# Kernel tuning notes

Hardware: AMD Instinct MI355X
Metric: run time of the kernel (lower is better)

Reference implementation:

```python
import jax, jax.numpy as jnp
import numpy as np
from jax import lax

K = 40
EPS = 1e-5
SLOPE = 0.2


def knn_idx(x, k):
    # x: (B, C, N); returns (B, N, k) indices of k nearest (L2), self included
    xx = jnp.sum(x * x, axis=1)                      # (B, N)
    inner = jnp.einsum('bcn,bcm->bnm', x, x)         # (B, N, N)
    dist = xx[:, :, None] - 2.0 * inner + xx[:, None, :]
    _, idx = lax.top_k(-dist, k)
    return idx


def get_graph_feature(x, k):
    # x: (B, C, N) -> (B, 2C, N, k)
    idx = knn_idx(x, k)
    xt = jnp.transpose(x, (0, 2, 1))                 # (B, N, C)
    feat = jax.vmap(lambda t, i: t[i])(xt, idx)      # (B, N, k, C)
    center = xt[:, :, None, :]                       # (B, N, 1, C)
    e = jnp.concatenate([feat - center, jnp.broadcast_to(center, feat.shape)], axis=-1)
    return jnp.transpose(e, (0, 3, 1, 2))            # (B, 2C, N, k)


def edge_block(x, W, gamma, beta, k):
    # EdgeConv: graph feature -> 1x1 conv -> BN(train-mode) -> LeakyReLU -> max over k
    e = get_graph_feature(x, k)                      # (B, 2C, N, k)
    y = jnp.einsum('oc,bcnk->bonk', W, e)            # (B, 32, N, k)
    m = jnp.mean(y, axis=(0, 2, 3), keepdims=True)
    v = jnp.mean((y - m) ** 2, axis=(0, 2, 3), keepdims=True)
    y = (y - m) / jnp.sqrt(v + EPS)
    y = y * gamma[None, :, None, None] + beta[None, :, None, None]
    y = jnp.where(y >= 0, y, SLOPE * y)
    return jnp.max(y, axis=-1)                       # (B, 32, N)


def setup_inputs() -> dict:
    key = jax.random.key(0)
    ks = jax.random.split(key, 16)
    B, C, N = 8, 9, 2048
    d = {
        'x': jax.random.normal(ks[0], (B, C, N), jnp.float32),
        'W1': jax.random.normal(ks[1], (32, 18), jnp.float32) * 0.1,
        'W2': jax.random.normal(ks[2], (32, 64), jnp.float32) * 0.1,
        'W3': jax.random.normal(ks[3], (32, 64), jnp.float32) * 0.1,
        'W4': jax.random.normal(ks[4], (32, 64), jnp.float32) * 0.1,
        'W5': jax.random.normal(ks[5], (128, 128), jnp.float32) * 0.1,
    }
    for i in range(4):
        d[f'g{i+1}'] = jnp.ones((32,), jnp.float32)
        d[f'b{i+1}'] = jnp.zeros((32,), jnp.float32)
    return d


def reference(x, W1, W2, W3, W4, W5, g1, g2, g3, g4, b1, b2, b3, b4):
    x1 = edge_block(x, W1, g1, b1, K)
    x2 = edge_block(x1, W2, g2, b2, K) + x1
    x3 = edge_block(x2, W3, g3, b3, K) + x2
    x4 = edge_block(x3, W4, g4, b4, K) + x3
    cat = jnp.concatenate([x1, x2, x3, x4], axis=1)  # (B, 128, N)
    return jnp.einsum('oc,bcn->bon', W5, cat)        # (B, 128, N)
```

## Files before the change

### kernel.cpp

```cpp
#include <hip/hip_runtime.h>
#include <stdint.h>

#define NP 2048
#define KNN 40
#define CAP 128

__device__ __forceinline__ unsigned fOrd(float f) {
    unsigned u = __float_as_uint(f);
    return u ^ ((unsigned)((int)u >> 31) | 0x80000000u);
}
__device__ __forceinline__ unsigned long long dOrd(double d) {
    unsigned long long u = (unsigned long long)__double_as_longlong(d);
    return u ^ (((unsigned long long)((long long)u >> 63)) | 0x8000000000000000ull);
}

template<int C, int CP, int CPX>
__global__ void prep_kernel(const float* __restrict__ X, long bstride,
                            const float* __restrict__ W,
                            float* __restrict__ p, float* __restrict__ r,
                            float* __restrict__ xx, float* __restrict__ XT) {
    __shared__ float wdT[C][32];
    __shared__ float wrT[C][32];
    int tid = threadIdx.x;
    for (int i = tid; i < 32 * C; i += 256) {
        int o = i / C, c = i - o * C;
        float wd = W[o * 2 * C + c];
        float wc = W[o * 2 * C + C + c];
        wdT[c][o] = wd;
        wrT[c][o] = wc - wd;
    }
    __syncthreads();
    int lane = tid & 63;
    int o = lane & 31;
    int h = lane >> 5;
    int wv = tid >> 6;
    int flat = blockIdx.x * 8 + wv * 2 + h;
    int b = flat >> 11, n = flat & 2047;
    const float* Xb = X + (long)b * bstride + n;
    float pacc = 0.f, racc = 0.f, xxa = 0.f, xto = 0.f;
    double xxd = 0.0;
#pragma unroll
    for (int c = 0; c < C; c++) {
        float xv = Xb[(long)c * NP];
        pacc = fmaf(wdT[c][o], xv, pacc);
        racc = fmaf(wrT[c][o], xv, racc);
        xxa += xv * xv;
        xxd += (double)xv * (double)xv;
        if (c == o) xto = xv;
    }
    long base = ((long)b * NP + n) * 32 + o;
    p[base] = pacc;
    r[base] = racc;
    long rowb = ((long)b * NP + n) * CPX;
    if (o < CP) XT[rowb + o] = (o < C) ? xto : 0.f;
    if (o == 0) {
        xx[b * NP + n] = xxa;
        *reinterpret_cast<double*>(&XT[rowb + CP]) = xxd;
    }
}

template<int C, int CP, int CPX>
__global__ __launch_bounds__(256, 2)
void knn_kernel(const float* __restrict__ X, long bstride,
                const float* __restrict__ p, const float* __restrict__ r,
                const float* __restrict__ xx, const float* __restrict__ XT,
                float* __restrict__ mmax, float* __restrict__ mmin,
                float* __restrict__ sums) {
    __shared__ __align__(16) float xt[2][C * 128];
    __shared__ __align__(16) float xxt[256];
    __shared__ __align__(8) float qld[4][CP][2];
    __shared__ int sel[8][KNN];
    __shared__ int cand[8][CAP];
    __shared__ float S1loc[32], S2loc[32];
    int tid = threadIdx.x;
    if (tid < 32) { S1loc[tid] = 0.f; S2loc[tid] = 0.f; }
    for (int i = tid; i < 8 * KNN; i += 256) ((int*)sel)[i] = 0;
    int lane = tid & 63;
    int wv = tid >> 6;
    int half = lane >> 5;
    int l32 = lane & 31;
    int b = blockIdx.x >> 8;
    int n0 = (blockIdx.x & 255) * 8;
    int nA = n0 + wv * 2, nB = nA + 1;
    int rowA = wv * 2, rowB = rowA + 1;
    const float* Xb = X + (long)b * bstride;
    const float* XTb = XT + (long)b * NP * CPX;
    long bNP = (long)b * NP;

    if (lane < CP) {
        qld[wv][lane][0] = XTb[(long)nA * CPX + lane];
        qld[wv][lane][1] = XTb[(long)nB * CPX + lane];
    }
    float xxnA = xx[bNP + nA];
    float xxnB = xx[bNP + nB];

    unsigned uA[16], uB[16];
    for (int t2 = 0; t2 < 8; t2++) {
        __syncthreads();
        for (int i = tid; i < C * 64; i += 256) {
            int c = i >> 6, g = i & 63;
            int tt = g >> 5, gg = g & 31;
            *(float4*)&xt[tt][c * 128 + gg * 4] =
                *(const float4*)&Xb[(long)c * NP + (t2 * 2 + tt) * 128 + gg * 4];
        }
        xxt[tid] = xx[bNP + t2 * 256 + tid];
        __syncthreads();
        const float* xth = xt[half];
        float4 ia = make_float4(0.f, 0.f, 0.f, 0.f);
        float4 ib = make_float4(0.f, 0.f, 0.f, 0.f);
#pragma unroll
        for (int c = 0; c < C; c++) {
            float2 q = *(const float2*)&qld[wv][c][0];
            float4 xv = *(const float4*)&xth[c * 128 + 4 * l32];
            ia.x = fmaf(q.x, xv.x, ia.x);
            ia.y = fmaf(q.x, xv.y, ia.y);
            ia.z = fmaf(q.x, xv.z, ia.z);
            ia.w = fmaf(q.x, xv.w, ia.w);
            ib.x = fmaf(q.y, xv.x, ib.x);
            ib.y = fmaf(q.y, xv.y, ib.y);
            ib.z = fmaf(q.y, xv.z, ib.z);
            ib.w = fmaf(q.y, xv.w, ib.w);
        }
        float4 xm = *(const float4*)&xxt[half * 128 + 4 * l32];
        unsigned a0 = fOrd((xxnA - 2.0f * ia.x) + xm.x) >> 16;
        unsigned a1 = fOrd((xxnA - 2.0f * ia.y) + xm.y) >> 16;
        unsigned a2 = fOrd((xxnA - 2.0f * ia.z) + xm.z) >> 16;
        unsigned a3 = fOrd((xxnA - 2.0f * ia.w) + xm.w) >> 16;
        unsigned b0 = fOrd((xxnB - 2.0f * ib.x) + xm.x) >> 16;
        unsigned b1 = fOrd((xxnB - 2.0f * ib.y) + xm.y) >> 16;
        unsigned b2_ = fOrd((xxnB - 2.0f * ib.z) + xm.z) >> 16;
        unsigned b3 = fOrd((xxnB - 2.0f * ib.w) + xm.w) >> 16;
        uA[2 * t2]     = (a1 << 16) | a0;
        uA[2 * t2 + 1] = (a3 << 16) | a2;
        uB[2 * t2]     = (b1 << 16) | b0;
        uB[2 * t2 + 1] = (b3 << 16) | b2_;
    }

    unsigned long long lmlt = (1ull << lane) - 1ull;

    double xxdA = *reinterpret_cast<const double*>(&XTb[(long)nA * CPX + CP]);
    double xxdB = *reinterpret_cast<const double*>(&XTb[(long)nB * CPX + CP]);

    unsigned vA = 0u, vB = 0u;
    for (int bit = 15; bit >= 0; bit--) {
        unsigned tA = vA | ((1u << bit) - 1u);
        unsigned tB = vB | ((1u << bit) - 1u);
        int cA = 0, cB = 0;
#pragma unroll
        for (int t = 0; t < 16; t++) {
            cA += __popcll(__ballot((uA[t] & 0xFFFFu) <= tA));
            cA += __popcll(__ballot((uA[t] >> 16) <= tA));
            cB += __popcll(__ballot((uB[t] & 0xFFFFu) <= tB));
            cB += __popcll(__ballot((uB[t] >> 16) <= tB));
        }
        if (cA < KNN) vA |= (1u << bit);
        if (cB < KNN) vB |= (1u << bit);
    }
    unsigned thrA = (vA > 0xFFFEu) ? 0xFFFFu : vA + 1u;
    unsigned thrB = (vB > 0xFFFEu) ? 0xFFFFu : vB + 1u;

    int baseA = 0, baseB = 0;
#pragma unroll
    for (int kk = 0; kk < 16; kk++) {
#pragma unroll
        for (int hh = 0; hh < 2; hh++) {
            unsigned kA = hh ? (uA[kk] >> 16) : (uA[kk] & 0xFFFFu);
            unsigned kB = hh ? (uB[kk] >> 16) : (uB[kk] & 0xFFFFu);
            int idx = (kk >> 1) * 256 + half * 128 + 4 * l32 + (kk & 1) * 2 + hh;
            bool pA = (kA <= thrA), pB = (kB <= thrB);
            unsigned long long mkA = __ballot(pA), mkB = __ballot(pB);
            if (pA) {
                int pos = baseA + __popcll(mkA & lmlt);
                if (pos < CAP) cand[rowA][pos] = idx;
            }
            if (pB) {
                int pos = baseB + __popcll(mkB & lmlt);
                if (pos < CAP) cand[rowB][pos] = idx;
            }
            baseA += __popcll(mkA);
            baseB += __popcll(mkB);
        }
    }
    int cntA = baseA < CAP ? baseA : CAP;
    int cntB = baseB < CAP ? baseB : CAP;

    unsigned long long keyA[CAP / 64], keyB[CAP / 64];
    int mixA[CAP / 64], mixB[CAP / 64];
#pragma unroll
    for (int s3 = 0; s3 < CAP / 64; s3++) {
        int slot = s3 * 64 + lane;
        keyA[s3] = ~0ull; mixA[s3] = 0;
        keyB[s3] = ~0ull; mixB[s3] = 0;
        if (slot < cntA) {
            int m = cand[rowA][slot] & (NP - 1);
            mixA[s3] = m;
            const float* xmp = XTb + (long)m * CPX;
            double inner = 0.0;
#pragma unroll
            for (int g = 0; g < CP / 4; g++) {
                float4 v = *(const float4*)&xmp[g * 4];
                inner += (double)qld[wv][g * 4 + 0][0] * (double)v.x;
                inner += (double)qld[wv][g * 4 + 1][0] * (double)v.y;
                inner += (double)qld[wv][g * 4 + 2][0] * (double)v.z;
                inner += (double)qld[wv][g * 4 + 3][0] * (double)v.w;
            }
            double xxm = *reinterpret_cast<const double*>(&xmp[CP]);
            double dd = (xxdA - 2.0 * inner) + xxm;
            keyA[s3] = dOrd(dd);
        }
        if (slot < cntB) {
            int m = cand[rowB][slot] & (NP - 1);
            mixB[s3] = m;
            const float* xmp = XTb + (long)m * CPX;
            double inner = 0.0;
#pragma unroll
            for (int g = 0; g < CP / 4; g++) {
                float4 v = *(const float4*)&xmp[g * 4];
                inner += (double)qld[wv][g * 4 + 0][1] * (double)v.x;
                inner += (double)qld[wv][g * 4 + 1][1] * (double)v.y;
                inner += (double)qld[wv][g * 4 + 2][1] * (double)v.z;
                inner += (double)qld[wv][g * 4 + 3][1] * (double)v.w;
            }
            double xxm = *reinterpret_cast<const double*>(&xmp[CP]);
            double dd = (xxdB - 2.0 * inner) + xxm;
            keyB[s3] = dOrd(dd);
        }
    }

    unsigned long long VA = 0ull, VB = 0ull;
    for (int bit = 62; bit >= 0; bit -= 2) {
        unsigned long long low = (1ull << bit) - 1ull;
        unsigned long long tA0 = VA | low;
        unsigned long long tA1 = VA | (1ull << bit) | low;
        unsigned long long tA2 = VA | (2ull << bit) | low;
        unsigned long long tB0 = VB | low;
        unsigned long long tB1 = VB | (1ull << bit) | low;
        unsigned long long tB2 = VB | (2ull << bit) | low;
        int cA0 = 0, cA1 = 0, cA2 = 0, cB0 = 0, cB1 = 0, cB2 = 0;
#pragma unroll
        for (int s3 = 0; s3 < CAP / 64; s3++) {
            cA0 += __popcll(__ballot(keyA[s3] <= tA0));
            cA1 += __popcll(__ballot(keyA[s3] <= tA1));
            cA2 += __popcll(__ballot(keyA[s3] <= tA2));
            cB0 += __popcll(__ballot(keyB[s3] <= tB0));
            cB1 += __popcll(__ballot(keyB[s3] <= tB1));
            cB2 += __popcll(__ballot(keyB[s3] <= tB2));
        }
        if (cA0 >= KNN) {  }
        else if (cA1 >= KNN) VA |= (1ull << bit);
        else if (cA2 >= KNN) VA |= (2ull << bit);
        else VA |= (3ull << bit);
        if (cB0 >= KNN) {  }
        else if (cB1 >= KNN) VB |= (1ull << bit);
        else if (cB2 >= KNN) VB |= (2ull << bit);
        else VB |= (3ull << bit);
    }

    int b2A = 0, b2B = 0;
#pragma unroll
    for (int s3 = 0; s3 < CAP / 64; s3++) {
        bool pA = (keyA[s3] < VA);
        bool pB = (keyB[s3] < VB);
        unsigned long long mkA = __ballot(pA), mkB = __ballot(pB);
        if (pA) {
            int pos = b2A + __popcll(mkA & lmlt);
            if (pos < KNN) sel[rowA][pos] = mixA[s3];
        }
        if (pB) {
            int pos = b2B + __popcll(mkB & lmlt);
            if (pos < KNN) sel[rowB][pos] = mixB[s3];
        }
        b2A += __popcll(mkA);
        b2B += __popcll(mkB);
    }
    {
        int needA = KNN - b2A;
        int needB = KNN - b2B;
        int tmA = 0, tmB = 0;
        for (int bit = 10; bit >= 0; bit--) {
            int tA = tmA | ((1 << bit) - 1);
            int tB = tmB | ((1 << bit) - 1);
            int cA = 0, cB = 0;
#pragma unroll
            for (int s3 = 0; s3 < CAP / 64; s3++) {
                cA += __popcll(__ballot(keyA[s3] == VA && mixA[s3] <= tA));
                cB += __popcll(__ballot(keyB[s3] == VB && mixB[s3] <= tB));
            }
            if (cA < needA) tmA |= (1 << bit);
            if (cB < needB) tmB |= (1 << bit);
        }
#pragma unroll
        for (int s3 = 0; s3 < CAP / 64; s3++) {
            bool pA = (keyA[s3] == VA && mixA[s3] <= tmA);
            bool pB = (keyB[s3] == VB && mixB[s3] <= tmB);
            unsigned long long mkA = __ballot(pA), mkB = __ballot(pB);
            if (pA) {
                int pos = b2A + __popcll(mkA & lmlt);
                if (pos < KNN) sel[rowA][pos] = mixA[s3];
            }
            if (pB) {
                int pos = b2B + __popcll(mkB & lmlt);
                if (pos < KNN) sel[rowB][pos] = mixB[s3];
            }
            b2A += __popcll(mkA);
            b2B += __popcll(mkB);
        }
    }

    {
        int o = lane & 31, h = lane >> 5;
        float s1A = 0.f, s2A = 0.f, s1B = 0.f, s2B = 0.f;
        float mxA = -__builtin_inff(), mnA = __builtin_inff();
        float mxB = -__builtin_inff(), mnB = __builtin_inff();
        const float* pb = p + bNP * 32 + o;
        for (int k = h * 20; k < h * 20 + 20; k++) {
            int mA = sel[rowA][k] & (NP - 1);
            int mB = sel[rowB][k] & (NP - 1);
            float pvA = pb[(long)mA * 32];
            float pvB = pb[(long)mB * 32];
            s1A += pvA;
            s2A = fmaf(pvA, pvA, s2A);
            mxA = fmaxf(mxA, pvA);
            mnA = fminf(mnA, pvA);
            s1B += pvB;
            s2B = fmaf(pvB, pvB, s2B);
            mxB = fmaxf(mxB, pvB);
            mnB = fminf(mnB, pvB);
        }
        s1A += __shfl_xor(s1A, 32);
        s2A += __shfl_xor(s2A, 32);
        mxA = fmaxf(mxA, __shfl_xor(mxA, 32));
        mnA = fminf(mnA, __shfl_xor(mnA, 32));
        s1B += __shfl_xor(s1B, 32);
        s2B += __shfl_xor(s2B, 32);
        mxB = fmaxf(mxB, __shfl_xor(mxB, 32));
        mnB = fminf(mnB, __shfl_xor(mnB, 32));
        if (h == 0) {
            long bseA = (bNP + nA) * 32 + o;
            float qA = r[bseA];
            mmax[bseA] = mxA + qA;
            mmin[bseA] = mnA + qA;
            atomicAdd(&S1loc[o], s1A + 40.f * qA);
            atomicAdd(&S2loc[o], fmaf(2.f * qA, s1A, fmaf(40.f * qA, qA, s2A)));
            long bseB = (bNP + nB) * 32 + o;
            float qB = r[bseB];
            mmax[bseB] = mxB + qB;
            mmin[bseB] = mnB + qB;
            atomicAdd(&S1loc[o], s1B + 40.f * qB);
            atomicAdd(&S2loc[o], fmaf(2.f * qB, s1B, fmaf(40.f * qB, qB, s2B)));
        }
    }
    __syncthreads();
    if (tid < 32) {
        atomicAdd(&sums[tid], S1loc[tid]);
        atomicAdd(&sums[32 + tid], S2loc[tid]);
    }
}

__global__ void finish_kernel(const float* __restrict__ mmax, const float* __restrict__ mmin,
                              const float* __restrict__ sums,
                              const float* __restrict__ g, const float* __restrict__ be,
                              const float* __restrict__ resid,
                              float* __restrict__ outb) {
    int id = blockIdx.x * 256 + threadIdx.x;
    int b = id >> 16;
    int o = (id >> 11) & 31;
    int n = id & 2047;
    const float cntf = 655360.0f;
    float mean = sums[o] / cntf;
    float var = sums[32 + o] / cntf - mean * mean;
    float sc = g[o] / sqrtf(var + 1e-5f);
    float sh = be[o] - mean * sc;
    long bse = ((long)b * NP + n) * 32 + o;
    float v = (sc >= 0.f) ? mmax[bse] : mmin[bse];
    float y = sc * v + sh;
    y = (y >= 0.f) ? y : 0.2f * y;
    long ob = ((long)b * 128 + o) * NP + n;
    if (resid) y += resid[ob];
    outb[ob] = y;
}

__global__ void final_gemm(const float* __restrict__ W5, float* __restrict__ out) {
    __shared__ __align__(16) float catL[128][32];
    int b = blockIdx.x >> 6;
    int n0 = (blockIdx.x & 63) * 32;
    int tid = threadIdx.x;
    for (int i = tid; i < 128 * 32; i += 256) {
        int c = i >> 5, nn = i & 31;
        catL[c][nn] = out[((long)b * 128 + c) * NP + n0 + nn];
    }
    __syncthreads();
    int og = tid >> 3, ng = tid & 7;
    int o0 = og * 4, nl = ng * 4;
    float acc[4][4] = {};
    for (int c = 0; c < 128; c++) {
        float4 cv = *(const float4*)&catL[c][nl];
#pragma unroll
        for (int i = 0; i < 4; i++) {
            float w = W5[(o0 + i) * 128 + c];
            acc[i][0] = fmaf(w, cv.x, acc[i][0]);
            acc[i][1] = fmaf(w, cv.y, acc[i][1]);
            acc[i][2] = fmaf(w, cv.z, acc[i][2]);
            acc[i][3] = fmaf(w, cv.w, acc[i][3]);
        }
    }
#pragma unroll
    for (int i = 0; i < 4; i++) {
        float4 vv = make_float4(acc[i][0], acc[i][1], acc[i][2], acc[i][3]);
        *(float4*)&out[((long)b * 128 + o0 + i) * NP + n0 + nl] = vv;
    }
}

extern "C" void kernel_launch(void* const* d_in, const int* in_sizes, int n_in,
                              void* d_out, int out_size, void* d_ws, size_t ws_size,
                              hipStream_t stream) {
    const float* x  = (const float*)d_in[0];
    const float* W1 = (const float*)d_in[1];
    const float* W2 = (const float*)d_in[2];
    const float* W3 = (const float*)d_in[3];
    const float* W4 = (const float*)d_in[4];
    const float* W5 = (const float*)d_in[5];
    const float* g1 = (const float*)d_in[6];
    const float* b1 = (const float*)d_in[7];
    const float* g2 = (const float*)d_in[8];
    const float* b2 = (const float*)d_in[9];
    const float* g3 = (const float*)d_in[10];
    const float* b3 = (const float*)d_in[11];
    const float* g4 = (const float*)d_in[12];
    const float* b4 = (const float*)d_in[13];
    float* out = (float*)d_out;
    float* ws  = (float*)d_ws;
    float* p    = ws;
    float* r    = ws + 524288;
    float* mmax = ws + 1048576;
    float* mmin = ws + 1572864;
    float* xx   = ws + 2097152;
    float* sums = ws + 2113536;
    float* XT   = ws + 2113792;
    hipMemsetAsync(sums, 0, 256 * sizeof(float), stream);

    prep_kernel<9, 12, 16><<<2048, 256, 0, stream>>>(x, 9L * NP, W1, p, r, xx, XT);
    knn_kernel<9, 12, 16><<<2048, 256, 0, stream>>>(x, 9L * NP, p, r, xx, XT, mmax, mmin, sums);
    finish_kernel<<<2048, 256, 0, stream>>>(mmax, mmin, sums, g1, b1, nullptr, out);
    const float* x1 = out;
    prep_kernel<32, 32, 36><<<2048, 256, 0, stream>>>(x1, 128L * NP, W2, p, r, xx, XT);
    knn_kernel<32, 32, 36><<<2048, 256, 0, stream>>>(x1, 128L * NP, p, r, xx, XT, mmax, mmin, sums + 64);
    finish_kernel<<<2048, 256, 0, stream>>>(mmax, mmin, sums + 64, g2, b2, x1, out + 32 * NP);
    const float* x2 = out + 32 * NP;
    prep_kernel<32, 32, 36><<<2048, 256, 0, stream>>>(x2, 128L * NP, W3, p, r, xx, XT);
    knn_kernel<32, 32, 36><<<2048, 256, 0, stream>>>(x2, 128L * NP, p, r, xx, XT, mmax, mmin, sums + 128);
    finish_kernel<<<2048, 256, 0, stream>>>(mmax, mmin, sums + 128, g3, b3, x2, out + 64 * NP);
    const float* x3 = out + 64 * NP;
    prep_kernel<32, 32, 36><<<2048, 256, 0, stream>>>(x3, 128L * NP, W4, p, r, xx, XT);
    knn_kernel<32, 32, 36><<<2048, 256, 0, stream>>>(x3, 128L * NP, p, r, xx, XT, mmax, mmin, sums + 192);
    finish_kernel<<<2048, 256, 0, stream>>>(mmax, mmin, sums + 192, g4, b4, x3, out + 96 * NP);

    final_gemm<<<512, 256, 0, stream>>>(W5, out);
}
```

Measured before the change: 728.5 us.

## Replace ballot-popcount counting with packed shuffle reductions and LDS atomic compaction

New measurement: 854.0 us. 17.2% more time.

```diff
diff --git a/kernel.cpp b/kernel.cpp
--- a/kernel.cpp
+++ b/kernel.cpp
@@ -12,6 +12,16 @@
 __device__ __forceinline__ unsigned long long dOrd(double d) {
     unsigned long long u = (unsigned long long)__double_as_longlong(d);
     return u ^ (((unsigned long long)((long long)u >> 63)) | 0x8000000000000000ull);
+}
+
+__device__ __forceinline__ unsigned wsum(unsigned pk) {
+    pk += __shfl_xor((int)pk, 1);
+    pk += __shfl_xor((int)pk, 2);
+    pk += __shfl_xor((int)pk, 4);
+    pk += __shfl_xor((int)pk, 8);
+    pk += __shfl_xor((int)pk, 16);
+    pk += __shfl_xor((int)pk, 32);
+    return pk;
 }
 
 template<int C, int CP, int CPX>
@@ -71,9 +81,12 @@
     __shared__ __align__(8) float qld[4][CP][2];
     __shared__ int sel[8][KNN];
     __shared__ int cand[8][CAP];
+    __shared__ int ccnt[8];
+    __shared__ int scnt[8];
     __shared__ float S1loc[32], S2loc[32];
     int tid = threadIdx.x;
     if (tid < 32) { S1loc[tid] = 0.f; S2loc[tid] = 0.f; }
+    if (tid < 8) { ccnt[tid] = 0; scnt[tid] = 0; }
     for (int i = tid; i < 8 * KNN; i += 256) ((int*)sel)[i] = 0;
     int lane = tid & 63;
     int wv = tid >> 6;
@@ -136,8 +149,6 @@
         uB[2 * t2 + 1] = (b3 << 16) | b2_;
     }
 
-    unsigned long long lmlt = (1ull << lane) - 1ull;
-
     double xxdA = *reinterpret_cast<const double*>(&XTb[(long)nA * CPX + CP]);
     double xxdB = *reinterpret_cast<const double*>(&XTb[(long)nB * CPX + CP]);
 
@@ -145,44 +156,37 @@
     for (int bit = 15; bit >= 0; bit--) {
         unsigned tA = vA | ((1u << bit) - 1u);
         unsigned tB = vB | ((1u << bit) - 1u);
-        int cA = 0, cB = 0;
-#pragma unroll
-        for (int t = 0; t < 16; t++) {
-            cA += __popcll(__ballot((uA[t] & 0xFFFFu) <= tA));
-            cA += __popcll(__ballot((uA[t] >> 16) <= tA));
-            cB += __popcll(__ballot((uB[t] & 0xFFFFu) <= tB));
-            cB += __popcll(__ballot((uB[t] >> 16) <= tB));
-        }
-        if (cA < KNN) vA |= (1u << bit);
-        if (cB < KNN) vB |= (1u << bit);
+        int cA0 = 0, cA1 = 0, cB0 = 0, cB1 = 0;
+#pragma unroll
+        for (int t = 0; t < 16; t += 2) {
+            unsigned ar0 = uA[t], ar1 = uA[t + 1];
+            unsigned br0 = uB[t], br1 = uB[t + 1];
+            cA0 += ((ar0 & 0xFFFFu) <= tA); cA0 += ((ar0 >> 16) <= tA);
+            cA1 += ((ar1 & 0xFFFFu) <= tA); cA1 += ((ar1 >> 16) <= tA);
+            cB0 += ((br0 & 0xFFFFu) <= tB); cB0 += ((br0 >> 16) <= tB);
+            cB1 += ((br1 & 0xFFFFu) <= tB); cB1 += ((br1 >> 16) <= tB);
+        }
+        unsigned pk = wsum((unsigned)(cA0 + cA1) | ((unsigned)(cB0 + cB1) << 16));
+        if ((pk & 0xFFFFu) < KNN) vA |= (1u << bit);
+        if ((pk >> 16) < KNN) vB |= (1u << bit);
     }
     unsigned thrA = (vA > 0xFFFEu) ? 0xFFFFu : vA + 1u;
     unsigned thrB = (vB > 0xFFFEu) ? 0xFFFFu : vB + 1u;
 
-    int baseA = 0, baseB = 0;
 #pragma unroll
     for (int kk = 0; kk < 16; kk++) {
-#pragma unroll
-        for (int hh = 0; hh < 2; hh++) {
-            unsigned kA = hh ? (uA[kk] >> 16) : (uA[kk] & 0xFFFFu);
-            unsigned kB = hh ? (uB[kk] >> 16) : (uB[kk] & 0xFFFFu);
-            int idx = (kk >> 1) * 256 + half * 128 + 4 * l32 + (kk & 1) * 2 + hh;
-            bool pA = (kA <= thrA), pB = (kB <= thrB);
-            unsigned long long mkA = __ballot(pA), mkB = __ballot(pB);
-            if (pA) {
-                int pos = baseA + __popcll(mkA & lmlt);
-                if (pos < CAP) cand[rowA][pos] = idx;
-            }
-            if (pB) {
-                int pos = baseB + __popcll(mkB & lmlt);
-                if (pos < CAP) cand[rowB][pos] = idx;
-            }
-            baseA += __popcll(mkA);
-            baseB += __popcll(mkB);
-        }
-    }
-    int cntA = baseA < CAP ? baseA : CAP;
-    int cntB = baseB < CAP ? baseB : CAP;
+        unsigned a = uA[kk], bb = uB[kk];
+        int idx = (kk >> 1) * 256 + half * 128 + 4 * l32 + (kk & 1) * 2;
+        if ((a & 0xFFFFu) <= thrA) { int q = atomicAdd(&ccnt[rowA], 1); if (q < CAP) cand[rowA][q] = idx; }
+        if ((a >> 16)     <= thrA) { int q = atomicAdd(&ccnt[rowA], 1); if (q < CAP) cand[rowA][q] = idx + 1; }
+        if ((bb & 0xFFFFu) <= thrB) { int q = atomicAdd(&ccnt[rowB], 1); if (q < CAP) cand[rowB][q] = idx; }
+        if ((bb >> 16)     <= thrB) { int q = atomicAdd(&ccnt[rowB], 1); if (q < CAP) cand[rowB][q] = idx + 1; }
+    }
+    int ra = 0, rb = 0;
+    if (lane == 0) ra = atomicAdd(&ccnt[rowA], 0);
+    if (lane == 1) rb = atomicAdd(&ccnt[rowB], 0);
+    int cntA = __shfl(ra, 0); cntA = cntA < CAP ? cntA : CAP;
+    int cntB = __shfl(rb, 1); cntB = cntB < CAP ? cntB : CAP;
 
     unsigned long long keyA[CAP / 64], keyB[CAP / 64];
     int mixA[CAP / 64], mixB[CAP / 64];
@@ -236,16 +240,19 @@
         unsigned long long tB0 = VB | low;
         unsigned long long tB1 = VB | (1ull << bit) | low;
         unsigned long long tB2 = VB | (2ull << bit) | low;
-        int cA0 = 0, cA1 = 0, cA2 = 0, cB0 = 0, cB1 = 0, cB2 = 0;
+        unsigned pA = 0, pB = 0;
 #pragma unroll
         for (int s3 = 0; s3 < CAP / 64; s3++) {
-            cA0 += __popcll(__ballot(keyA[s3] <= tA0));
-            cA1 += __popcll(__ballot(keyA[s3] <= tA1));
-            cA2 += __popcll(__ballot(keyA[s3] <= tA2));
-            cB0 += __popcll(__ballot(keyB[s3] <= tB0));
-            cB1 += __popcll(__ballot(keyB[s3] <= tB1));
-            cB2 += __popcll(__ballot(keyB[s3] <= tB2));
-        }
+            pA += (unsigned)(keyA[s3] <= tA0);
+            pA += (unsigned)(keyA[s3] <= tA1) << 10;
+            pA += (unsigned)(keyA[s3] <= tA2) << 20;
+            pB += (unsigned)(keyB[s3] <= tB0);
+            pB += (unsigned)(keyB[s3] <= tB1) << 10;
+            pB += (unsigned)(keyB[s3] <= tB2) << 20;
+        }
+        pA = wsum(pA); pB = wsum(pB);
+        int cA0 = pA & 1023, cA1 = (pA >> 10) & 1023, cA2 = pA >> 20;
+        int cB0 = pB & 1023, cB1 = (pB >> 10) & 1023, cB2 = pB >> 20;
         if (cA0 >= KNN) {  }
         else if (cA1 >= KNN) VA |= (1ull << bit);
         else if (cA2 >= KNN) VA |= (2ull << bit);
@@ -256,54 +263,36 @@
         else VB |= (3ull << bit);
     }
 
-    int b2A = 0, b2B = 0;
-#pragma unroll
-    for (int s3 = 0; s3 < CAP / 64; s3++) {
-        bool pA = (keyA[s3] < VA);
-        bool pB = (keyB[s3] < VB);
-        unsigned long long mkA = __ballot(pA), mkB = __ballot(pB);
-        if (pA) {
-            int pos = b2A + __popcll(mkA & lmlt);
-            if (pos < KNN) sel[rowA][pos] = mixA[s3];
-        }
-        if (pB) {
-            int pos = b2B + __popcll(mkB & lmlt);
-            if (pos < KNN) sel[rowB][pos] = mixB[s3];
-        }
-        b2A += __popcll(mkA);
-        b2B += __popcll(mkB);
-    }
     {
-        int needA = KNN - b2A;
-        int needB = KNN - b2B;
+        unsigned ps = 0;
+#pragma unroll
+        for (int s3 = 0; s3 < CAP / 64; s3++) {
+            ps += (unsigned)(keyA[s3] < VA);
+            ps += (unsigned)(keyB[s3] < VB) << 16;
+        }
+        ps = wsum(ps);
+        int needA = KNN - (int)(ps & 0xFFFFu);
+        int needB = KNN - (int)(ps >> 16);
         int tmA = 0, tmB = 0;
         for (int bit = 10; bit >= 0; bit--) {
             int tA = tmA | ((1 << bit) - 1);
             int tB = tmB | ((1 << bit) - 1);
-            int cA = 0, cB = 0;
+            unsigned pk = 0;
 #pragma unroll
             for (int s3 = 0; s3 < CAP / 64; s3++) {
-                cA += __popcll(__ballot(keyA[s3] == VA && mixA[s3] <= tA));
-                cB += __popcll(__ballot(keyB[s3] == VB && mixB[s3] <= tB));
+                pk += (unsigned)(keyA[s3] == VA && mixA[s3] <= tA);
+                pk += (unsigned)(keyB[s3] == VB && mixB[s3] <= tB) << 16;
             }
-            if (cA < needA) tmA |= (1 << bit);
-            if (cB < needB) tmB |= (1 << bit);
+            pk = wsum(pk);
+            if ((int)(pk & 0xFFFFu) < needA) tmA |= (1 << bit);
+            if ((int)(pk >> 16) < needB) tmB |= (1 << bit);
         }
 #pragma unroll
         for (int s3 = 0; s3 < CAP / 64; s3++) {
-            bool pA = (keyA[s3] == VA && mixA[s3] <= tmA);
-            bool pB = (keyB[s3] == VB && mixB[s3] <= tmB);
-            unsigned long long mkA = __ballot(pA), mkB = __ballot(pB);
-            if (pA) {
-                int pos = b2A + __popcll(mkA & lmlt);
-                if (pos < KNN) sel[rowA][pos] = mixA[s3];
-            }
-            if (pB) {
-                int pos = b2B + __popcll(mkB & lmlt);
-                if (pos < KNN) sel[rowB][pos] = mixB[s3];
-            }
-            b2A += __popcll(mkA);
-            b2B += __popcll(mkB);
+            bool pAo = (keyA[s3] < VA) || (keyA[s3] == VA && mixA[s3] <= tmA);
+            bool pBo = (keyB[s3] < VB) || (keyB[s3] == VB && mixB[s3] <= tmB);
+            if (pAo) { int q = atomicAdd(&scnt[rowA], 1); if (q < KNN) sel[rowA][q] = mixA[s3]; }
+            if (pBo) { int q = atomicAdd(&scnt[rowB], 1); if (q < KNN) sel[rowB][q] = mixB[s3]; }
         }
     }
 
```

## Replace radix threshold search with wavefront bitonic sort for top-k selection

Applied to the files above, without the earlier changes.

Measured after the change: 683.0 us. 1.07x faster.

```diff
diff --git a/kernel.cpp b/kernel.cpp
--- a/kernel.cpp
+++ b/kernel.cpp
@@ -227,84 +227,68 @@
         }
     }
 
-    unsigned long long VA = 0ull, VB = 0ull;
-    for (int bit = 62; bit >= 0; bit -= 2) {
-        unsigned long long low = (1ull << bit) - 1ull;
-        unsigned long long tA0 = VA | low;
-        unsigned long long tA1 = VA | (1ull << bit) | low;
-        unsigned long long tA2 = VA | (2ull << bit) | low;
-        unsigned long long tB0 = VB | low;
-        unsigned long long tB1 = VB | (1ull << bit) | low;
-        unsigned long long tB2 = VB | (2ull << bit) | low;
-        int cA0 = 0, cA1 = 0, cA2 = 0, cB0 = 0, cB1 = 0, cB2 = 0;
-#pragma unroll
-        for (int s3 = 0; s3 < CAP / 64; s3++) {
-            cA0 += __popcll(__ballot(keyA[s3] <= tA0));
-            cA1 += __popcll(__ballot(keyA[s3] <= tA1));
-            cA2 += __popcll(__ballot(keyA[s3] <= tA2));
-            cB0 += __popcll(__ballot(keyB[s3] <= tB0));
-            cB1 += __popcll(__ballot(keyB[s3] <= tB1));
-            cB2 += __popcll(__ballot(keyB[s3] <= tB2));
-        }
-        if (cA0 >= KNN) {  }
-        else if (cA1 >= KNN) VA |= (1ull << bit);
-        else if (cA2 >= KNN) VA |= (2ull << bit);
-        else VA |= (3ull << bit);
-        if (cB0 >= KNN) {  }
-        else if (cB1 >= KNN) VB |= (1ull << bit);
-        else if (cB2 >= KNN) VB |= (2ull << bit);
-        else VB |= (3ull << bit);
-    }
-
-    int b2A = 0, b2B = 0;
-#pragma unroll
-    for (int s3 = 0; s3 < CAP / 64; s3++) {
-        bool pA = (keyA[s3] < VA);
-        bool pB = (keyB[s3] < VB);
-        unsigned long long mkA = __ballot(pA), mkB = __ballot(pB);
-        if (pA) {
-            int pos = b2A + __popcll(mkA & lmlt);
-            if (pos < KNN) sel[rowA][pos] = mixA[s3];
-        }
-        if (pB) {
-            int pos = b2B + __popcll(mkB & lmlt);
-            if (pos < KNN) sel[rowB][pos] = mixB[s3];
-        }
-        b2A += __popcll(mkA);
-        b2B += __popcll(mkB);
-    }
-    {
-        int needA = KNN - b2A;
-        int needB = KNN - b2B;
-        int tmA = 0, tmB = 0;
-        for (int bit = 10; bit >= 0; bit--) {
-            int tA = tmA | ((1 << bit) - 1);
-            int tB = tmB | ((1 << bit) - 1);
-            int cA = 0, cB = 0;
-#pragma unroll
-            for (int s3 = 0; s3 < CAP / 64; s3++) {
-                cA += __popcll(__ballot(keyA[s3] == VA && mixA[s3] <= tA));
-                cB += __popcll(__ballot(keyB[s3] == VB && mixB[s3] <= tB));
-            }
-            if (cA < needA) tmA |= (1 << bit);
-            if (cB < needB) tmB |= (1 << bit);
-        }
-#pragma unroll
-        for (int s3 = 0; s3 < CAP / 64; s3++) {
-            bool pA = (keyA[s3] == VA && mixA[s3] <= tmA);
-            bool pB = (keyB[s3] == VB && mixB[s3] <= tmB);
-            unsigned long long mkA = __ballot(pA), mkB = __ballot(pB);
-            if (pA) {
-                int pos = b2A + __popcll(mkA & lmlt);
-                if (pos < KNN) sel[rowA][pos] = mixA[s3];
-            }
-            if (pB) {
-                int pos = b2B + __popcll(mkB & lmlt);
-                if (pos < KNN) sel[rowB][pos] = mixB[s3];
-            }
-            b2A += __popcll(mkA);
-            b2B += __popcll(mkB);
-        }
+    auto cex = [](unsigned long long& k, int& i, const int S, const bool keepmin) {
+        unsigned long long pk = __shfl_xor(k, S);
+        int pi = __shfl_xor(i, S);
+        bool less = (k < pk) || (k == pk && i < pi);
+        bool tp = (less != keepmin);
+        k = tp ? pk : k;
+        i = tp ? pi : i;
+    };
+    if (cntA <= 64 && cntB <= 64) {
+#pragma unroll
+        for (int kk2 = 1; kk2 <= 6; kk2++) {
+            const int K = 1 << kk2;
+#pragma unroll
+            for (int ss = kk2 - 1; ss >= 0; ss--) {
+                const int S = 1 << ss;
+                bool asc0 = (K == 64) ? true : ((lane & K) == 0);
+                bool km0 = ((lane & S) == 0) == asc0;
+                cex(keyA[0], mixA[0], S, km0);
+                cex(keyB[0], mixB[0], S, km0);
+            }
+        }
+    } else {
+#pragma unroll
+        for (int kk2 = 1; kk2 <= 6; kk2++) {
+            const int K = 1 << kk2;
+#pragma unroll
+            for (int ss = kk2 - 1; ss >= 0; ss--) {
+                const int S = 1 << ss;
+                bool ascL = (lane & K) == 0;
+                bool asc0 = (K == 64) ? true  : ascL;
+                bool asc1 = (K == 64) ? false : ascL;
+                bool km0 = ((lane & S) == 0) == asc0;
+                bool km1 = ((lane & S) == 0) == asc1;
+                cex(keyA[0], mixA[0], S, km0);
+                cex(keyA[1], mixA[1], S, km1);
+                cex(keyB[0], mixB[0], S, km0);
+                cex(keyB[1], mixB[1], S, km1);
+            }
+        }
+        {
+            bool lA = (keyA[0] < keyA[1]) || (keyA[0] == keyA[1] && mixA[0] < mixA[1]);
+            unsigned long long tk = keyA[0]; int ti = mixA[0];
+            keyA[0] = lA ? keyA[0] : keyA[1];  mixA[0] = lA ? mixA[0] : mixA[1];
+            keyA[1] = lA ? keyA[1] : tk;       mixA[1] = lA ? mixA[1] : ti;
+            bool lB = (keyB[0] < keyB[1]) || (keyB[0] == keyB[1] && mixB[0] < mixB[1]);
+            tk = keyB[0]; ti = mixB[0];
+            keyB[0] = lB ? keyB[0] : keyB[1];  mixB[0] = lB ? mixB[0] : mixB[1];
+            keyB[1] = lB ? keyB[1] : tk;       mixB[1] = lB ? mixB[1] : ti;
+        }
+#pragma unroll
+        for (int ss = 5; ss >= 0; ss--) {
+            const int S = 1 << ss;
+            bool km = ((lane & S) == 0);
+            cex(keyA[0], mixA[0], S, km);
+            cex(keyA[1], mixA[1], S, km);
+            cex(keyB[0], mixB[0], S, km);
+            cex(keyB[1], mixB[1], S, km);
+        }
+    }
+    if (lane < KNN) {
+        sel[rowA][lane] = mixA[0];
+        sel[rowB][lane] = mixB[0];
     }
 
     {
```
